# Optimization experiments

Hardware: AMD Instinct MI355X
Metric: run time of the kernel (lower is better)

The kernel has to match this reference:

```python
import jax, jax.numpy as jnp
import numpy as np

# Graph / model dims (match init_kwargs config)
N1, N2, N3 = 80000, 16000, 4096
E1, E2 = 256000, 65536
D_IN, H1, C1 = 256, 8, 64   # conv1: concat -> 512
H2, C2 = 4, 64              # conv2: mean over heads -> gnn_outdim=64
F_IN, F_HID, L_DIM, N_CLS = 128, 64, 64, 1


def setup_inputs() -> dict:
    key = jax.random.key(0)
    ks = jax.random.split(key, 20)
    rng = np.random.default_rng(0)

    def edges(E, n_src, n_dst):
        src = rng.integers(0, n_src, size=E)
        dst = rng.integers(0, n_dst, size=E)
        # avoid incidental self loops (PyG remove_self_loops); explicit ones added in conv
        src = np.where(src == dst, src + 1, src)
        return jnp.asarray(src, jnp.int32), jnp.asarray(dst, jnp.int32)

    es1, ed1 = edges(E1, N1, N2)
    es2, ed2 = edges(E2, N2, N3)
    s = 0.05
    return {
        "x": jax.random.normal(ks[0], (N1, D_IN), jnp.float32),
        "flat": jax.random.normal(ks[1], (N3, F_IN), jnp.float32),
        "last": jax.random.normal(ks[2], (N3, L_DIM), jnp.float32),
        "edge_src1": es1, "edge_dst1": ed1,
        "edge_src2": es2, "edge_dst2": ed2,
        "W1_src": jax.random.normal(ks[3], (D_IN, H1 * C1), jnp.float32) * s,
        "W1_dst": jax.random.normal(ks[4], (D_IN, H1 * C1), jnp.float32) * s,
        "att1_src": jax.random.normal(ks[5], (H1, C1), jnp.float32) * s,
        "att1_dst": jax.random.normal(ks[6], (H1, C1), jnp.float32) * s,
        "bias1": jax.random.normal(ks[7], (H1 * C1,), jnp.float32) * s,
        "W2_src": jax.random.normal(ks[8], (H1 * C1, H2 * C2), jnp.float32) * s,
        "W2_dst": jax.random.normal(ks[9], (H1 * C1, H2 * C2), jnp.float32) * s,
        "att2_src": jax.random.normal(ks[10], (H2, C2), jnp.float32) * s,
        "att2_dst": jax.random.normal(ks[11], (H2, C2), jnp.float32) * s,
        "bias2": jax.random.normal(ks[12], (C2,), jnp.float32) * s,
        "flat_W": jax.random.normal(ks[13], (F_IN, F_HID), jnp.float32) * s,
        "flat_b": jax.random.normal(ks[14], (F_HID,), jnp.float32) * s,
        "out_W": jax.random.normal(ks[15], (C2 + F_HID + L_DIM, N_CLS), jnp.float32) * s,
        "out_b": jax.random.normal(ks[16], (N_CLS,), jnp.float32) * s,
    }


def gat_conv(x_src, x_dst, src, dst, W_s, W_d, a_s, a_d, b, concat):
    """PyG bipartite GATConv (eval mode, add_self_loops=True, neg slope 0.2)."""
    H, C = a_s.shape
    Ns, Nd = x_src.shape[0], x_dst.shape[0]
    h_s = (x_src @ W_s).reshape(Ns, H, C)
    h_d = (x_dst @ W_d).reshape(Nd, H, C)
    sl = jnp.arange(Nd, dtype=src.dtype)
    src = jnp.concatenate([src, sl])  # self loops on target nodes
    dst = jnp.concatenate([dst, sl])
    e_s = jnp.einsum("nhc,hc->nh", h_s, a_s)  # [Ns,H]
    e_d = jnp.einsum("nhc,hc->nh", h_d, a_d)  # [Nd,H]
    alpha = jax.nn.leaky_relu(e_s[src] + e_d[dst], negative_slope=0.2)  # [E,H]
    amax = jax.ops.segment_max(alpha, dst, num_segments=Nd)[dst]
    ex = jnp.exp(alpha - amax)
    w = ex / jax.ops.segment_sum(ex, dst, num_segments=Nd)[dst]  # segment softmax
    msg = w[:, :, None] * h_s[src]  # [E,H,C]
    out = jax.ops.segment_sum(msg, dst, num_segments=Nd)  # [Nd,H,C]
    out = out.reshape(Nd, H * C) if concat else out.mean(axis=1)
    return out + b


def reference(x, flat, last, edge_src1, edge_dst1, edge_src2, edge_dst2,
              W1_src, W1_dst, att1_src, att1_dst, bias1,
              W2_src, W2_dst, att2_src, att2_dst, bias2,
              flat_W, flat_b, out_W, out_b):
    # eval mode: featdrop / attndrop / main_dropout are identity
    h = gat_conv(x, x[:N2], edge_src1, edge_dst1,
                 W1_src, W1_dst, att1_src, att1_dst, bias1, concat=True)
    h = jax.nn.elu(h)
    h = gat_conv(h, h[:N3], edge_src2, edge_dst2,
                 W2_src, W2_dst, att2_src, att2_dst, bias2, concat=False)
    f = flat @ flat_W + flat_b
    z = jnp.concatenate([h, f, last], axis=1)  # [N3, 64+64+64]
    return z @ out_W + out_b  # [N3, num_cls]
```

## Files before the change

kernel.cpp:

```cpp
#include <hip/hip_runtime.h>
#include <hip/hip_bf16.h>
#include <cstdio>

typedef __attribute__((ext_vector_type(8))) short short8;
typedef __attribute__((ext_vector_type(8))) _Float16 half8;
typedef __attribute__((ext_vector_type(2))) __fp16 fp16x2;
typedef __attribute__((ext_vector_type(4))) float f32x4;
typedef __attribute__((ext_vector_type(4))) unsigned int uint4v;
typedef __attribute__((ext_vector_type(2))) unsigned int uint2v;

#if defined(__has_builtin)
#if __has_builtin(__builtin_amdgcn_fdot2) && __has_builtin(__builtin_amdgcn_perm) && __has_builtin(__builtin_amdgcn_cvt_pkrtz)
#define USE_DOT2 1
#endif
#endif

__device__ __forceinline__ float bfu2f(unsigned short u) {
    return __uint_as_float(((unsigned)u) << 16);
}
__device__ __forceinline__ unsigned short f2bfu(float f) {
    __hip_bfloat16 b = __float2bfloat16(f);
    union { __hip_bfloat16 b; unsigned short u; } cv; cv.b = b;
    return cv.u;
}
__device__ __forceinline__ unsigned short f2hu(float f) {
    _Float16 h = (_Float16)f;
    union { _Float16 h; unsigned short u; } cv; cv.h = h;
    return cv.u;
}
__device__ __forceinline__ float hu2f(unsigned short u) {
    union { unsigned short u; _Float16 h; } cv; cv.u = u;
    return (float)cv.h;
}
#ifdef USE_DOT2
__device__ __forceinline__ unsigned pkw(float w0, float w1) {
    union { fp16x2 v; unsigned u; } cv;
    cv.v = __builtin_amdgcn_cvt_pkrtz(w0, w1);
    return cv.u;
}
__device__ __forceinline__ float fdot2acc(unsigned a, unsigned b, float c) {
    union { unsigned u; fp16x2 v; } ua, ub; ua.u = a; ub.u = b;
    return __builtin_amdgcn_fdot2(ua.v, ub.v, c, false);
}
#endif

#define N1 80000
#define N2 16000
#define N3 4096
#define E1 256000
#define E2 65536

__global__ void prep_hist(const float* __restrict__ W1s, unsigned short* __restrict__ w1s_pk,
                          const float* __restrict__ W2s, unsigned short* __restrict__ w2s_pk,
                          const float* __restrict__ W1d, const float* __restrict__ a1d,
                          float* __restrict__ v1dT,
                          const float* __restrict__ W2d, const float* __restrict__ a2d,
                          float* __restrict__ v2dT,
                          const float* __restrict__ fW, unsigned short* __restrict__ fw_t3,
                          int PB,
                          const int* __restrict__ ed1i, int* __restrict__ cnt1,
                          const int* __restrict__ ed2i, int* __restrict__ cnt2) {
    const int bid = blockIdx.x;
    if (bid < PB) {
        int i = bid * 256 + threadIdx.x;
        const int S0 = 131072, S1 = 131072, S2 = 8192;
        if (i < S0) {
            int k = i >> 9, n = i & 511;
            int n16 = n >> 4, l = n & 15, k32 = k >> 5, qq = (k >> 3) & 3, e = k & 7;
            size_t base = ((size_t)(n16 * 8 + k32)) * 512 + (qq * 16 + l) * 8 + e;
            w1s_pk[base] = f2hu(W1s[i]);
        } else if (i < S0 + S1) {
            int j = i - S0;
            int k = j >> 8, n = j & 255;
            int n16 = n >> 4, l = n & 15, k32 = k >> 5, qq = (k >> 3) & 3, e = k & 7;
            size_t base = ((size_t)(n16 * 16 + k32)) * 512 + (qq * 16 + l) * 8 + e;
            w2s_pk[base] = f2hu(W2s[j]);
        } else if (i < S0 + S1 + S2) {
            int j = i - S0 - S1;
            int k = j >> 6, n = j & 63;
            float v = fW[j];
            unsigned short h = f2bfu(v);
            unsigned short l = f2bfu(v - bfu2f(h));
            size_t base = (size_t)n * 384;
            fw_t3[base + k] = h;
            fw_t3[base + 128 + k] = l;
            fw_t3[base + 256 + k] = h;
        } else {
            int j = i - S0 - S1 - S2;
            if (j < 2048) {
                int h = j >> 8, k = j & 255;
                float s = 0.f;
                for (int c = 0; c < 64; c++) s += W1d[k * 512 + h * 64 + c] * a1d[h * 64 + c];
                v1dT[j] = s;
            } else if (j < 4096) {
                int jj = j - 2048;
                int h = jj >> 9, k = jj & 511;
                float s = 0.f;
                for (int c = 0; c < 64; c++) s += W2d[k * 256 + h * 64 + c] * a2d[h * 64 + c];
                v2dT[jj] = s;
            }
        }
    } else {
        int i = (bid - PB) * 256 + threadIdx.x;
        if (i < E1) {
            int d = ed1i[i];
            if ((unsigned)d < (unsigned)N2) atomicAdd(&cnt1[d], 1);
        } else if (i < E1 + E2) {
            int d = ed2i[i - E1];
            if ((unsigned)d < (unsigned)N3) atomicAdd(&cnt2[d], 1);
        }
    }
}

__global__ __launch_bounds__(1024)
void scan_dual(const int* __restrict__ c1, int* __restrict__ s1, int Nd1,
               const int* __restrict__ c2, int* __restrict__ s2, int Nd2) {
    const int* cnt = (blockIdx.x == 0) ? c1 : c2;
    int* start = (blockIdx.x == 0) ? s1 : s2;
    int Nd = (blockIdx.x == 0) ? Nd1 : Nd2;
    __shared__ int part[1024];
    int t = threadIdx.x;
    int k = (Nd + 1023) >> 10;
    int lo = t * k, hi = min(lo + k, Nd);
    if (lo > Nd) lo = Nd;
    int s = 0;
    for (int i = lo; i < hi; i++) s += cnt[i];
    part[t] = s;
    __syncthreads();
    for (int off = 1; off < 1024; off <<= 1) {
        int v = (t >= off) ? part[t - off] : 0;
        __syncthreads();
        part[t] += v;
        __syncthreads();
    }
    int run = (t > 0) ? part[t - 1] : 0;
    for (int i = lo; i < hi; i++) { start[i] = run; run += cnt[i]; }
    if (t == 1023) start[Nd] = part[1023];
}

__device__ __forceinline__ void fill_core(int fb,
        const int* __restrict__ sa1, const int* __restrict__ da1,
        const int* __restrict__ st1, int* __restrict__ cu1, int* __restrict__ cs1,
        const int* __restrict__ sa2, const int* __restrict__ da2,
        const int* __restrict__ st2, int* __restrict__ cu2, int* __restrict__ cs2) {
    int i = fb * 256 + threadIdx.x;
    const int *sa, *da, *st;
    int *cu, *cs;
    int Nd, Ns, e;
    if (i < E1) { sa = sa1; da = da1; st = st1; cu = cu1; cs = cs1; Nd = N2; Ns = N1; e = i; }
    else if (i < E1 + E2) { sa = sa2; da = da2; st = st2; cu = cu2; cs = cs2; Nd = N3; Ns = N2; e = i - E1; }
    else return;
    int d = da[e];
    if ((unsigned)d >= (unsigned)Nd) return;
    int p = atomicAdd(&cu[d], 1);
    int idx = st[d] + p;
    if (idx >= st[d + 1]) return;
    int s = sa[e];
    if ((unsigned)s >= (unsigned)Ns) s = 0;
    cs[idx] = s;
}

__device__ __forceinline__ void ed1_core(const float* __restrict__ x, const float* __restrict__ v1dT,
                                         float* __restrict__ ed1, int blk) {
    const int lane = threadIdx.x & 63;
    const int w = threadIdx.x >> 6;
    float4 vv[8];
#pragma unroll
    for (int h = 0; h < 8; h++) vv[h] = *(const float4*)&v1dT[h * 256 + lane * 4];
    for (int i = 0; i < 4; i++) {
        int d = blk * 16 + w * 4 + i;
        if (d >= N2) return;
        float4 xv = *(const float4*)&x[(size_t)d * 256 + lane * 4];
        float p[8];
#pragma unroll
        for (int h = 0; h < 8; h++)
            p[h] = xv.x * vv[h].x + xv.y * vv[h].y + xv.z * vv[h].z + xv.w * vv[h].w;
#pragma unroll
        for (int off = 1; off < 64; off <<= 1)
#pragma unroll
            for (int h = 0; h < 8; h++) p[h] += __shfl_xor(p[h], off);
        if (lane < 8) {
            int hh = lane;
            float a01 = (hh & 1) ? p[1] : p[0], a23 = (hh & 1) ? p[3] : p[2];
            float a45 = (hh & 1) ? p[5] : p[4], a67 = (hh & 1) ? p[7] : p[6];
            float b0 = (hh & 2) ? a23 : a01, b1 = (hh & 2) ? a67 : a45;
            ed1[d * 8 + hh] = (hh & 4) ? b1 : b0;
        }
    }
}
__device__ __forceinline__ void ed2_core(const unsigned short* __restrict__ xh,
                                         const float* __restrict__ v2dT,
                                         float* __restrict__ ed2, int blk) {
    const int lane = threadIdx.x & 63;
    const int w = threadIdx.x >> 6;
    float vv[4][8];
#pragma unroll
    for (int h = 0; h < 4; h++)
#pragma unroll
        for (int j = 0; j < 8; j++) vv[h][j] = v2dT[h * 512 + lane * 8 + j];
    for (int i = 0; i < 4; i++) {
        int d = blk * 16 + w * 4 + i;
        if (d >= N3) return;
        uint4v rw = *(const uint4v*)&xh[(size_t)d * 512 + lane * 8];
        const unsigned short* rb = (const unsigned short*)&rw;
        float xf[8];
#pragma unroll
        for (int j = 0; j < 8; j++) xf[j] = hu2f(rb[j]);
        float p[4];
#pragma unroll
        for (int h = 0; h < 4; h++) {
            float s = 0.f;
#pragma unroll
            for (int j = 0; j < 8; j++) s += xf[j] * vv[h][j];
            p[h] = s;
        }
#pragma unroll
        for (int off = 1; off < 64; off <<= 1)
#pragma unroll
            for (int h = 0; h < 4; h++) p[h] += __shfl_xor(p[h], off);
        if (lane < 4) {
            int hh = lane;
            float a01 = (hh & 1) ? p[1] : p[0], a23 = (hh & 1) ? p[3] : p[2];
            ed2[d * 4 + hh] = (hh & 2) ? a23 : a01;
        }
    }
}

template <bool AF16>
__device__ __forceinline__ void gemm_core(_Float16 (*As)[64][72],
              const void* __restrict__ Ax,
              const unsigned short* __restrict__ Bp, unsigned short* __restrict__ C,
              const float* __restrict__ att, float* __restrict__ es_out,
              int MT, int NB, int N, int K, int H, int hb) {
    const int xcd = hb & 7;
    const int sI = hb >> 3;
    const int mt = (sI / NB) * 8 + xcd;
    const int nb = sI % NB;
    if (mt >= MT) return;
    const int m0 = mt * 64;
    const int tid = threadIdx.x;
    const int wave = tid >> 6, lane = tid & 63;
    const int q = lane >> 4, l15 = lane & 15;
    const int n0 = nb * 256 + wave * 64;
    const int KS = K >> 6;
    const int KSB = K >> 5;
    const int arow = tid >> 2, ac16 = (tid & 3) * 16;
    const unsigned short* Bbase = Bp + (size_t)(n0 >> 4) * KSB * 512 + lane * 8;

    f32x4 acc[4][4] = {};
    half8 b[2][4];
    float4 s0, s1, s2, s3;
    half8 sh0, sh1;

    auto stageLoad = [&](int t) {
        if constexpr (AF16) {
            const _Float16* p = (const _Float16*)Ax + (size_t)(m0 + arow) * K + t * 64 + ac16;
            sh0 = *(const half8*)p;
            sh1 = *(const half8*)(p + 8);
        } else {
            const float* p = (const float*)Ax + (size_t)(m0 + arow) * K + t * 64 + ac16;
            s0 = *(const float4*)p;
            s1 = *(const float4*)(p + 4);
            s2 = *(const float4*)(p + 8);
            s3 = *(const float4*)(p + 12);
        }
    };
    auto stageWrite = [&](int buf) {
        half8 v0, v1;
        if constexpr (AF16) {
            v0 = sh0; v1 = sh1;
        } else {
            v0[0] = (_Float16)s0.x; v0[1] = (_Float16)s0.y;
            v0[2] = (_Float16)s0.z; v0[3] = (_Float16)s0.w;
            v0[4] = (_Float16)s1.x; v0[5] = (_Float16)s1.y;
            v0[6] = (_Float16)s1.z; v0[7] = (_Float16)s1.w;
            v1[0] = (_Float16)s2.x; v1[1] = (_Float16)s2.y;
            v1[2] = (_Float16)s2.z; v1[3] = (_Float16)s2.w;
            v1[4] = (_Float16)s3.x; v1[5] = (_Float16)s3.y;
            v1[6] = (_Float16)s3.z; v1[7] = (_Float16)s3.w;
        }
        *(half8*)&As[buf][arow][ac16] = v0;
        *(half8*)&As[buf][arow][ac16 + 8] = v1;
    };
    auto loadB = [&](int k32, int kh, int nt) {
        b[kh][nt] = *(const half8*)(Bbase + ((size_t)nt * KSB + k32) * 512);
    };

    stageLoad(0);
#pragma unroll
    for (int kh = 0; kh < 2; kh++)
#pragma unroll
        for (int nt = 0; nt < 4; nt++) loadB(kh, kh, nt);
    stageWrite(0);
    __syncthreads();

    int cur = 0;
    for (int t = 0; t < KS; t++) {
        const bool hn = (t + 1) < KS;
        if (hn) stageLoad(t + 1);
#pragma unroll
        for (int kh = 0; kh < 2; kh++) {
#pragma unroll
            for (int rg = 0; rg < 4; rg++) {
                half8 a = *(const half8*)&As[cur][rg * 16 + l15][kh * 32 + q * 8];
#pragma unroll
                for (int nt = 0; nt < 4; nt++) {
                    acc[rg][nt] = __builtin_amdgcn_mfma_f32_16x16x32_f16(a, b[kh][nt], acc[rg][nt], 0, 0, 0);
                    if (rg == 3 && hn) loadB(2 * (t + 1) + kh, kh, nt);
                }
            }
        }
        if (hn) {
            stageWrite(cur ^ 1);
            __syncthreads();
        }
        cur ^= 1;
    }

#pragma unroll
    for (int rg = 0; rg < 4; rg++)
#pragma unroll
        for (int nt = 0; nt < 4; nt++)
#pragma unroll
            for (int r = 0; r < 4; r++) {
                int row = m0 + rg * 16 + q * 4 + r;
                int col = n0 + nt * 16 + l15;
                C[(size_t)row * N + col] = f2hu(acc[rg][nt][r]);
            }
    {
        const int head = n0 >> 6;
        float av[4];
#pragma unroll
        for (int nt = 0; nt < 4; nt++) av[nt] = att[head * 64 + nt * 16 + l15];
#pragma unroll
        for (int rg = 0; rg < 4; rg++)
#pragma unroll
            for (int r = 0; r < 4; r++) {
                float p = acc[rg][0][r] * av[0] + acc[rg][1][r] * av[1]
                        + acc[rg][2][r] * av[2] + acc[rg][3][r] * av[3];
#pragma unroll
                for (int off = 1; off < 16; off <<= 1) p += __shfl_xor(p, off);
                if (l15 == 0)
                    es_out[(size_t)(m0 + rg * 16 + q * 4 + r) * H + head] = p;
            }
    }
}

__global__ __launch_bounds__(256, 2)
void gemm1_fused(const void* __restrict__ Ax,
                 const unsigned short* __restrict__ Bp, unsigned short* __restrict__ C,
                 const float* __restrict__ att, float* __restrict__ es_out,
                 int MT, int NB, int N, int K, int H, int G1, int FB,
                 const int* sa1, const int* da1, const int* st1, int* cu1, int* cs1,
                 const int* sa2, const int* da2, const int* st2, int* cu2, int* cs2,
                 const float* __restrict__ xe, const float* __restrict__ v1dT,
                 float* __restrict__ ed1) {
    __shared__ alignas(16) _Float16 As[2][64][72];
    const int bid = blockIdx.x;
    if (bid < G1) gemm_core<false>(As, Ax, Bp, C, att, es_out, MT, NB, N, K, H, bid);
    else if (bid < G1 + FB) fill_core(bid - G1, sa1, da1, st1, cu1, cs1, sa2, da2, st2, cu2, cs2);
    else ed1_core(xe, v1dT, ed1, bid - G1 - FB);
}

__device__ __forceinline__ void flat_core(unsigned char* smemraw,
        const float* __restrict__ A, const unsigned short* __restrict__ Bt3,
        float* __restrict__ C, int mb) {
    const int K = 128, N = 64, KK = 384;
    auto As = (unsigned short (*)[64][72])smemraw;
    auto Bs = (unsigned short (*)[72])(smemraw + 18432);
    const int tid = threadIdx.x;
    const int wave = tid >> 6, lane = tid & 63;
    const int wr = wave >> 1, wc = wave & 1;
    const int quad = lane >> 4, l15 = lane & 15;
    const int m0 = mb * 64, n0 = 0;
    f32x4 acc[2][2] = {};
    for (int k0 = 0; k0 < KK; k0 += 64) {
        const int seg = k0 / K;
        const int ks = k0 - seg * K;
#pragma unroll
        for (int i = 0; i < 2; i++) {
            int idx = tid + i * 256;
            int r = idx >> 3, cv = (idx & 7) * 8;
            const float* ap = &A[(size_t)(m0 + r) * K + ks + cv];
            const float4 v0 = *(const float4*)ap;
            const float4 v1 = *(const float4*)(ap + 4);
            float va[8] = {v0.x, v0.y, v0.z, v0.w, v1.x, v1.y, v1.z, v1.w};
            short8 h8, l8;
#pragma unroll
            for (int j = 0; j < 8; j++) {
                unsigned short hh = f2bfu(va[j]);
                h8[j] = (short)hh;
                l8[j] = (short)f2bfu(va[j] - bfu2f(hh));
            }
            *(short8*)&As[0][r][cv] = h8;
            *(short8*)&As[1][r][cv] = l8;
            *(short8*)&Bs[r][cv] = *(const short8*)&Bt3[(size_t)(n0 + r) * KK + k0 + cv];
        }
        __syncthreads();
        const int abank = (seg < 2) ? 0 : 1;
#pragma unroll
        for (int kk = 0; kk < 64; kk += 32) {
            short8 a[2], b[2];
#pragma unroll
            for (int t = 0; t < 2; t++) {
                a[t] = *(const short8*)&As[abank][wr * 32 + t * 16 + l15][kk + quad * 8];
                b[t] = *(const short8*)&Bs[wc * 32 + t * 16 + l15][kk + quad * 8];
            }
#pragma unroll
            for (int mt = 0; mt < 2; mt++)
#pragma unroll
                for (int nt = 0; nt < 2; nt++)
                    acc[mt][nt] = __builtin_amdgcn_mfma_f32_16x16x32_bf16(
                        a[mt], b[nt], acc[mt][nt], 0, 0, 0);
        }
        __syncthreads();
    }
#pragma unroll
    for (int mt = 0; mt < 2; mt++)
#pragma unroll
        for (int nt = 0; nt < 2; nt++)
#pragma unroll
            for (int r = 0; r < 4; r++) {
                int row = m0 + wr * 32 + mt * 16 + quad * 4 + r;
                int col = n0 + wc * 32 + nt * 16 + l15;
                C[(size_t)row * N + col] = acc[mt][nt][r];
            }
}

__global__ __launch_bounds__(256, 2)
void gemm2_fused(const void* __restrict__ Ax,
                 const unsigned short* __restrict__ Bp, unsigned short* __restrict__ C,
                 const float* __restrict__ att, float* __restrict__ es_out,
                 int MT, int NB, int N, int K, int H, int G2, int FLB,
                 const float* __restrict__ fA, const unsigned short* __restrict__ fBt3,
                 float* __restrict__ fC,
                 const unsigned short* __restrict__ x2h, const float* __restrict__ v2dT,
                 float* __restrict__ ed2) {
    __shared__ alignas(16) unsigned char smem[27648];
    const int bid = blockIdx.x;
    if (bid < G2) gemm_core<true>((_Float16(*)[64][72])smem, Ax, Bp, C, att, es_out,
                                  MT, NB, N, K, H, bid);
    else if (bid < G2 + FLB) flat_core(smem, fA, fBt3, fC, bid - G2);
    else ed2_core(x2h, v2dT, ed2, bid - G2 - FLB);
}

template <int H, bool ELU, bool HOUT, bool FIN>
__global__ __launch_bounds__(256)
void gat_agg3(const int* __restrict__ csr, const int* __restrict__ rs,
              const unsigned short* __restrict__ hs,
              const float* __restrict__ es,
              const float* __restrict__ edv,
              const float* __restrict__ bias,
              void* __restrict__ out, int Nd,
              const float* __restrict__ fbuf, const float* __restrict__ flat_b,
              const float* __restrict__ last, const float* __restrict__ outW,
              const float* __restrict__ outb, float* __restrict__ fout) {
    constexpr int LH = (H == 8) ? 3 : 2;
    constexpr int EPC = 64 >> LH;
    constexpr int ND = H / 2;
    const int lane = threadIdx.x & 63;
    const int d = blockIdx.x * 4 + (threadIdx.x >> 6);
    if (d >= Nd) return;
    const int h = lane & (H - 1);
    const int e0 = lane >> LH;
    const int hB = lane >> (6 - LH);
    const float edh = edv[(size_t)d * H + h];
    const int beg = rs[d];
    const int deg = rs[d + 1] - beg;
    const int n = deg + 1;
    const int nch = (n + EPC - 1) / EPC;
    float acc[H] = {};
    const size_t rowoff = (size_t)lane * H;
    if (nch <= 8) {
        int idxA = d, idxB = d;
        if (lane < deg) idxA = csr[beg + lane];
        if constexpr (H == 4) { if (64 + lane < deg) idxB = csr[beg + 64 + lane]; }
        float av[8];
#pragma unroll
        for (int c = 0; c < 8; c++) {
            if (c < nch) {
                int jv = c * EPC + e0;
                int s;
                if (c * EPC + EPC - 1 < 64) s = __shfl(idxA, jv);
                else s = __shfl(idxB, jv - 64);
                av[c] = es[(size_t)s * H + h];
            }
        }
        unsigned rvA[EPC][ND], rvB[EPC][ND];
        auto loadChunk = [&](int c, unsigned (&rv)[EPC][ND]) {
#pragma unroll
            for (int u = 0; u < EPC; u++) {
                int src = c * EPC + u;
                int s = (src < 64) ? __shfl(idxA, src) : __shfl(idxB, src - 64);
                const unsigned short* rp = &hs[(size_t)s * (H * 64) + rowoff];
                if constexpr (H == 8) *(uint4v*)&rv[u][0] = *(const uint4v*)rp;
                else *(uint2v*)&rv[u][0] = *(const uint2v*)rp;
            }
        };
        loadChunk(0, rvA);
        float al[8], mx = -1e30f;
#pragma unroll
        for (int c = 0; c < 8; c++) {
            int jv = c * EPC + e0;
            float a = -1e30f;
            if (c < nch && jv < n) { a = av[c] + edh; a = (a > 0.f) ? a : 0.2f * a; }
            al[c] = a;
            mx = fmaxf(mx, a);
        }
#pragma unroll
        for (int off = H; off < 64; off <<= 1) mx = fmaxf(mx, __shfl_xor(mx, off));
        float exv[8], den = 0.f;
#pragma unroll
        for (int c = 0; c < 8; c++) { exv[c] = expf(al[c] - mx); den += exv[c]; }
#pragma unroll
        for (int off = H; off < 64; off <<= 1) den += __shfl_xor(den, off);
        const float inv = 1.f / den;
        float ec[8];
#pragma unroll
        for (int c = 0; c < 8; c++) ec[c] = exv[c] * inv;
        auto computeChunk = [&](int c, unsigned (&rv)[EPC][ND]) {
#pragma unroll
            for (int pu = 0; pu < EPC / 2; pu++) {
                float w0 = __shfl(ec[c], (2 * pu) * H + hB);
                float w1 = __shfl(ec[c], (2 * pu + 1) * H + hB);
#ifdef USE_DOT2
                unsigned w2 = pkw(w0, w1);
#pragma unroll
                for (int dwi = 0; dwi < ND; dwi++) {
                    unsigned lo = __builtin_amdgcn_perm(rv[2 * pu + 1][dwi], rv[2 * pu][dwi], 0x05040100u);
                    unsigned hi = __builtin_amdgcn_perm(rv[2 * pu + 1][dwi], rv[2 * pu][dwi], 0x07060302u);
                    acc[2 * dwi] = fdot2acc(w2, lo, acc[2 * dwi]);
                    acc[2 * dwi + 1] = fdot2acc(w2, hi, acc[2 * dwi + 1]);
                }
#else
#pragma unroll
                for (int dwi = 0; dwi < ND; dwi++) {
                    unsigned q0 = rv[2 * pu][dwi], q1 = rv[2 * pu + 1][dwi];
                    acc[2 * dwi]     += w0 * hu2f((unsigned short)(q0 & 0xffff))
                                      + w1 * hu2f((unsigned short)(q1 & 0xffff));
                    acc[2 * dwi + 1] += w0 * hu2f((unsigned short)(q0 >> 16))
                                      + w1 * hu2f((unsigned short)(q1 >> 16));
                }
#endif
            }
        };
#pragma unroll
        for (int c = 0; c < 8; c += 2) {
            if (c >= nch) break;
            if (c + 1 < nch) loadChunk(c + 1, rvB);
            computeChunk(c, rvA);
            if (c + 1 >= nch) break;
            if (c + 2 < nch) loadChunk(c + 2, rvA);
            computeChunk(c + 1, rvB);
        }
    } else {
        float mx = -1e30f;
        for (int j0 = 0; j0 < n; j0 += EPC) {
            int j = j0 + e0;
            if (j < n) {
                int s = (j < deg) ? csr[beg + j] : d;
                float a = es[(size_t)s * H + h] + edh;
                a = (a > 0.0f) ? a : 0.2f * a;
                mx = fmaxf(mx, a);
            }
        }
#pragma unroll
        for (int off = H; off < 64; off <<= 1) mx = fmaxf(mx, __shfl_xor(mx, off));
        float den = 0.0f;
        for (int j0 = 0; j0 < n; j0 += EPC) {
            int j = j0 + e0;
            if (j < n) {
                int s = (j < deg) ? csr[beg + j] : d;
                float a = es[(size_t)s * H + h] + edh;
                a = (a > 0.0f) ? a : 0.2f * a;
                den += expf(a - mx);
            }
        }
#pragma unroll
        for (int off = H; off < 64; off <<= 1) den += __shfl_xor(den, off);
        const float inv = 1.0f / den;
        const float mB = __shfl(mx, hB);
        const float invB = __shfl(inv, hB);
        const float edhB = __shfl(edh, hB);
        for (int j = 0; j < n; j++) {
            int s = (j < deg) ? csr[beg + j] : d;
            const unsigned short* rp = &hs[(size_t)s * (H * 64) + rowoff];
            float a = es[(size_t)s * H + hB] + edhB;
            a = (a > 0.0f) ? a : 0.2f * a;
            float w = expf(a - mB) * invB;
#pragma unroll
            for (int k = 0; k < H; k++) acc[k] += w * hu2f(rp[k]);
        }
    }
    if constexpr (FIN) {
        float f4[4];
#pragma unroll
        for (int k = 0; k < 4; k++) {
            float a2v = acc[k] + __shfl_xor(acc[k], 32);
            f4[k] = a2v + __shfl_xor(a2v, 16);
        }
        float part = 0.f;
        if (lane < 16) {
            const int c0 = lane * 4;
            float4 fb4 = *(const float4*)&fbuf[(size_t)d * 64 + c0];
            float4 lb4 = *(const float4*)&last[(size_t)d * 64 + c0];
            const float* fbv = &fb4.x;
            const float* lbv = &lb4.x;
#pragma unroll
            for (int k = 0; k < 4; k++) {
                int c = c0 + k;
                float h2 = 0.25f * f4[k] + bias[c];
                part += h2 * outW[c];
                part += (fbv[k] + flat_b[c]) * outW[64 + c];
                part += lbv[k] * outW[128 + c];
            }
        }
#pragma unroll
        for (int off = 1; off < 16; off <<= 1) part += __shfl_xor(part, off);
        if (lane == 0) fout[d] = part + outb[0];
    } else {
#pragma unroll
        for (int k = 0; k < H; k++) {
            float v = acc[k];
            if (ELU) {
                v += bias[lane * H + k];
                v = (v > 0.0f) ? v : expm1f(v);
            }
            acc[k] = v;
        }
        if constexpr (HOUT) {
            half8 hv;
#pragma unroll
            for (int k = 0; k < H; k++) hv[k] = (_Float16)acc[k];
            _Float16* op = (_Float16*)out + (size_t)d * (H * 64) + rowoff;
            *(half8*)op = hv;
        } else {
            float* op = (float*)out + (size_t)d * (H * 64) + rowoff;
#pragma unroll
            for (int qd = 0; qd < H / 4; qd++)
                *(float4*)&op[qd * 4] = *(float4*)&acc[qd * 4];
        }
    }
}

extern "C" void kernel_launch(void* const* d_in, const int* in_sizes, int n_in,
                              void* d_out, int out_size, void* d_ws, size_t ws_size,
                              hipStream_t stream) {
    const float* x    = (const float*)d_in[0];
    const float* flat = (const float*)d_in[1];
    const float* last = (const float*)d_in[2];
    const int*  es1i  = (const int*)d_in[3];
    const int*  ed1i  = (const int*)d_in[4];
    const int*  es2i  = (const int*)d_in[5];
    const int*  ed2i  = (const int*)d_in[6];
    const float* W1s  = (const float*)d_in[7];
    const float* W1d  = (const float*)d_in[8];
    const float* a1s  = (const float*)d_in[9];
    const float* a1d  = (const float*)d_in[10];
    const float* b1   = (const float*)d_in[11];
    const float* W2s  = (const float*)d_in[12];
    const float* W2d  = (const float*)d_in[13];
    const float* a2s  = (const float*)d_in[14];
    const float* a2d  = (const float*)d_in[15];
    const float* b2   = (const float*)d_in[16];
    const float* fW   = (const float*)d_in[17];
    const float* fb   = (const float*)d_in[18];
    const float* oW   = (const float*)d_in[19];
    const float* ob   = (const float*)d_in[20];
    float* out = (float*)d_out;

    float* ws = (float*)d_ws;
    unsigned short* hs1_h = (unsigned short*)ws;
    float* es1f = ws + 24576000;
    float* ed1f = ws + 25216000;
    float* acc1 = ws + 25344000;
    unsigned short* wb = (unsigned short*)(ws + 54016000);
    unsigned short* w1s_pk = wb;
    unsigned short* w2s_pk = wb + 524288;
    unsigned short* fw_t3  = wb + 1048576;
    float* v1dT = ws + 54600000;
    float* v2dT = ws + 54602048;
    int* ibase   = (int*)(ws + 54816000);
    int* cnt1    = ibase;
    int* cursor1 = ibase + 16000;
    int* cnt2    = ibase + 32000;
    int* cursor2 = ibase + 36096;
    int* start1  = ibase + 40192;
    int* start2  = ibase + 56193;
    int* csr1    = ibase + 60290;
    int* csr2    = ibase + 316290;
    const size_t NEED = ((size_t)54816000 + 381826) * 4;
    if (ws_size < NEED) {
        fprintf(stderr, "kernel_launch: ws_size %zu < needed %zu\n", ws_size, NEED);
        return;
    }
    unsigned short* hs2_h = (unsigned short*)ws;
    float* es2f = ws + 2572288;
    float* ed2f = ws + 2636288;
    float* fbuf = ws + 3701248;
    unsigned short* acc1h = (unsigned short*)acc1;

    (void)hipMemsetAsync(ibase, 0, 40192 * sizeof(int), stream);
    {
        const int PB = 1072;
        const int HB = (E1 + E2) / 256;
        prep_hist<<<PB + HB, 256, 0, stream>>>(
            W1s, w1s_pk, W2s, w2s_pk,
            W1d, a1d, v1dT, W2d, a2d, v2dT,
            fW, fw_t3, PB, ed1i, cnt1, ed2i, cnt2);
    }
    scan_dual<<<2, 1024, 0, stream>>>(cnt1, start1, N2, cnt2, start2, N3);

    {
        const int MT = N1 / 64;
        const int NB = 2;
        const int G1 = 8 * NB * ((MT + 7) / 8);
        const int FB = (E1 + E2) / 256;
        const int EB = N2 / 16;
        gemm1_fused<<<G1 + FB + EB, 256, 0, stream>>>(
            x, w1s_pk, hs1_h, a1s, es1f, MT, NB, 512, 256, 8, G1, FB,
            es1i, ed1i, start1, cursor1, csr1, es2i, ed2i, start2, cursor2, csr2,
            x, v1dT, ed1f);
    }
    gat_agg3<8, true, true, false><<<N2 / 4, 256, 0, stream>>>(
        csr1, start1, hs1_h, es1f, ed1f, b1, acc1h, N2,
        nullptr, nullptr, nullptr, nullptr, nullptr, nullptr);

    {
        const int MT = N2 / 64;
        const int G2 = 8 * ((MT + 7) / 8);
        const int FLB = N3 / 64;
        const int EB2 = N3 / 16;
        gemm2_fused<<<G2 + FLB + EB2, 256, 0, stream>>>(
            acc1h, w2s_pk, hs2_h, a2s, es2f, MT, 1, 256, 512, 4, G2, FLB,
            flat, fw_t3, fbuf,
            acc1h, v2dT, ed2f);
    }
    gat_agg3<4, false, false, true><<<N3 / 4, 256, 0, stream>>>(
        csr2, start2, hs2_h, es2f, ed2f, b2, nullptr, N3,
        fbuf, fb, last, oW, ob, out);
}
```

Before: 322.4 us.

## Stage full-K A tile in LDS once and loop N passes per block

The GEMM core now loads the entire K-depth A tile into shared memory once, replacing the double-buffered K-step pipeline. For gemm1, one block computes both 256-column halves in two passes over the resident A tile, so x is read and converted once instead of by two blocks. For gemm2, the M tile shrinks to 32 rows with full K=512 resident, doubling block count. This removes redundant A reads and per-step barriers, but loses overlap of global loads with MFMA and increases LDS use, which may lower occupancy.

After: 326.3 us. No clear change (+1.2%).

```diff
diff --git a/kernel.cpp b/kernel.cpp
--- a/kernel.cpp
+++ b/kernel.cpp
@@ -226,123 +226,113 @@
     }
 }
 
-template <bool AF16>
-__device__ __forceinline__ void gemm_core(_Float16 (*As)[64][72],
+template <bool AF16, int MR, int KDIM, int NPASS, int PAD>
+__device__ __forceinline__ void gemm_core(_Float16* Ast,
               const void* __restrict__ Ax,
               const unsigned short* __restrict__ Bp, unsigned short* __restrict__ C,
               const float* __restrict__ att, float* __restrict__ es_out,
-              int MT, int NB, int N, int K, int H, int hb) {
+              int MT, int N, int H, int hb) {
+    constexpr int RG = MR / 16;
+    constexpr int KS = KDIM / 64;
+    constexpr int KSB = KDIM / 32;
     const int xcd = hb & 7;
-    const int sI = hb >> 3;
-    const int mt = (sI / NB) * 8 + xcd;
-    const int nb = sI % NB;
+    const int mt = (hb >> 3) * 8 + xcd;
     if (mt >= MT) return;
-    const int m0 = mt * 64;
+    const int m0 = mt * MR;
     const int tid = threadIdx.x;
     const int wave = tid >> 6, lane = tid & 63;
     const int q = lane >> 4, l15 = lane & 15;
-    const int n0 = nb * 256 + wave * 64;
-    const int KS = K >> 6;
-    const int KSB = K >> 5;
-    const int arow = tid >> 2, ac16 = (tid & 3) * 16;
-    const unsigned short* Bbase = Bp + (size_t)(n0 >> 4) * KSB * 512 + lane * 8;
-
-    f32x4 acc[4][4] = {};
-    half8 b[2][4];
-    float4 s0, s1, s2, s3;
-    half8 sh0, sh1;
-
-    auto stageLoad = [&](int t) {
-        if constexpr (AF16) {
-            const _Float16* p = (const _Float16*)Ax + (size_t)(m0 + arow) * K + t * 64 + ac16;
-            sh0 = *(const half8*)p;
-            sh1 = *(const half8*)(p + 8);
-        } else {
-            const float* p = (const float*)Ax + (size_t)(m0 + arow) * K + t * 64 + ac16;
-            s0 = *(const float4*)p;
-            s1 = *(const float4*)(p + 4);
-            s2 = *(const float4*)(p + 8);
-            s3 = *(const float4*)(p + 12);
-        }
-    };
-    auto stageWrite = [&](int buf) {
-        half8 v0, v1;
-        if constexpr (AF16) {
-            v0 = sh0; v1 = sh1;
-        } else {
-            v0[0] = (_Float16)s0.x; v0[1] = (_Float16)s0.y;
-            v0[2] = (_Float16)s0.z; v0[3] = (_Float16)s0.w;
-            v0[4] = (_Float16)s1.x; v0[5] = (_Float16)s1.y;
-            v0[6] = (_Float16)s1.z; v0[7] = (_Float16)s1.w;
-            v1[0] = (_Float16)s2.x; v1[1] = (_Float16)s2.y;
-            v1[2] = (_Float16)s2.z; v1[3] = (_Float16)s2.w;
-            v1[4] = (_Float16)s3.x; v1[5] = (_Float16)s3.y;
-            v1[6] = (_Float16)s3.z; v1[7] = (_Float16)s3.w;
-        }
-        *(half8*)&As[buf][arow][ac16] = v0;
-        *(half8*)&As[buf][arow][ac16 + 8] = v1;
-    };
-    auto loadB = [&](int k32, int kh, int nt) {
-        b[kh][nt] = *(const half8*)(Bbase + ((size_t)nt * KSB + k32) * 512);
-    };
-
-    stageLoad(0);
-#pragma unroll
-    for (int kh = 0; kh < 2; kh++)
-#pragma unroll
-        for (int nt = 0; nt < 4; nt++) loadB(kh, kh, nt);
-    stageWrite(0);
+
+    if constexpr (!AF16) {
+        const int srow = tid >> 2, scg = (tid & 3) * 64;
+        const float* sp = (const float*)Ax + (size_t)(m0 + srow) * KDIM + scg;
+        _Float16* dp = &Ast[srow * PAD + scg];
+#pragma unroll
+        for (int r = 0; r < 4; r++) {
+            float4 v0 = *(const float4*)(sp + r * 16);
+            float4 v1 = *(const float4*)(sp + r * 16 + 4);
+            float4 v2 = *(const float4*)(sp + r * 16 + 8);
+            float4 v3 = *(const float4*)(sp + r * 16 + 12);
+            half8 h0, h1;
+            h0[0] = (_Float16)v0.x; h0[1] = (_Float16)v0.y;
+            h0[2] = (_Float16)v0.z; h0[3] = (_Float16)v0.w;
+            h0[4] = (_Float16)v1.x; h0[5] = (_Float16)v1.y;
+            h0[6] = (_Float16)v1.z; h0[7] = (_Float16)v1.w;
+            h1[0] = (_Float16)v2.x; h1[1] = (_Float16)v2.y;
+            h1[2] = (_Float16)v2.z; h1[3] = (_Float16)v2.w;
+            h1[4] = (_Float16)v3.x; h1[5] = (_Float16)v3.y;
+            h1[6] = (_Float16)v3.z; h1[7] = (_Float16)v3.w;
+            *(half8*)(dp + r * 16) = h0;
+            *(half8*)(dp + r * 16 + 8) = h1;
+        }
+    } else {
+        const int srow = tid >> 3, scg = (tid & 7) * 64;
+        const _Float16* sp = (const _Float16*)Ax + (size_t)(m0 + srow) * KDIM + scg;
+        _Float16* dp = &Ast[srow * PAD + scg];
+#pragma unroll
+        for (int r = 0; r < 4; r++) {
+            half8 h0 = *(const half8*)(sp + r * 16);
+            half8 h1 = *(const half8*)(sp + r * 16 + 8);
+            *(half8*)(dp + r * 16) = h0;
+            *(half8*)(dp + r * 16 + 8) = h1;
+        }
+    }
     __syncthreads();
 
-    int cur = 0;
-    for (int t = 0; t < KS; t++) {
-        const bool hn = (t + 1) < KS;
-        if (hn) stageLoad(t + 1);
-#pragma unroll
-        for (int kh = 0; kh < 2; kh++) {
-#pragma unroll
-            for (int rg = 0; rg < 4; rg++) {
-                half8 a = *(const half8*)&As[cur][rg * 16 + l15][kh * 32 + q * 8];
-#pragma unroll
-                for (int nt = 0; nt < 4; nt++) {
-                    acc[rg][nt] = __builtin_amdgcn_mfma_f32_16x16x32_f16(a, b[kh][nt], acc[rg][nt], 0, 0, 0);
-                    if (rg == 3 && hn) loadB(2 * (t + 1) + kh, kh, nt);
+#pragma unroll
+    for (int np = 0; np < NPASS; np++) {
+        const int n0 = np * 256 + wave * 64;
+        const unsigned short* Bbase = Bp + (size_t)(n0 >> 4) * KSB * 512 + lane * 8;
+        f32x4 acc[RG][4] = {};
+        half8 b[2][4];
+        auto loadB = [&](int k32, int kh, int nt) {
+            b[kh][nt] = *(const half8*)(Bbase + ((size_t)nt * KSB + k32) * 512);
+        };
+#pragma unroll
+        for (int kh = 0; kh < 2; kh++)
+#pragma unroll
+            for (int nt = 0; nt < 4; nt++) loadB(kh, kh, nt);
+#pragma unroll
+        for (int t = 0; t < KS; t++) {
+#pragma unroll
+            for (int kh = 0; kh < 2; kh++)
+#pragma unroll
+                for (int rg = 0; rg < RG; rg++) {
+                    half8 a = *(const half8*)&Ast[(rg * 16 + l15) * PAD + t * 64 + kh * 32 + q * 8];
+#pragma unroll
+                    for (int nt = 0; nt < 4; nt++) {
+                        acc[rg][nt] = __builtin_amdgcn_mfma_f32_16x16x32_f16(a, b[kh][nt], acc[rg][nt], 0, 0, 0);
+                        if (rg == RG - 1 && t + 1 < KS) loadB(2 * (t + 1) + kh, kh, nt);
+                    }
                 }
-            }
-        }
-        if (hn) {
-            stageWrite(cur ^ 1);
-            __syncthreads();
-        }
-        cur ^= 1;
-    }
-
-#pragma unroll
-    for (int rg = 0; rg < 4; rg++)
-#pragma unroll
-        for (int nt = 0; nt < 4; nt++)
-#pragma unroll
-            for (int r = 0; r < 4; r++) {
-                int row = m0 + rg * 16 + q * 4 + r;
-                int col = n0 + nt * 16 + l15;
-                C[(size_t)row * N + col] = f2hu(acc[rg][nt][r]);
-            }
-    {
-        const int head = n0 >> 6;
-        float av[4];
-#pragma unroll
-        for (int nt = 0; nt < 4; nt++) av[nt] = att[head * 64 + nt * 16 + l15];
-#pragma unroll
-        for (int rg = 0; rg < 4; rg++)
-#pragma unroll
-            for (int r = 0; r < 4; r++) {
-                float p = acc[rg][0][r] * av[0] + acc[rg][1][r] * av[1]
-                        + acc[rg][2][r] * av[2] + acc[rg][3][r] * av[3];
-#pragma unroll
-                for (int off = 1; off < 16; off <<= 1) p += __shfl_xor(p, off);
-                if (l15 == 0)
-                    es_out[(size_t)(m0 + rg * 16 + q * 4 + r) * H + head] = p;
-            }
+        }
+#pragma unroll
+        for (int rg = 0; rg < RG; rg++)
+#pragma unroll
+            for (int nt = 0; nt < 4; nt++)
+#pragma unroll
+                for (int r = 0; r < 4; r++) {
+                    int row = m0 + rg * 16 + q * 4 + r;
+                    int col = n0 + nt * 16 + l15;
+                    C[(size_t)row * N + col] = f2hu(acc[rg][nt][r]);
+                }
+        {
+            const int head = n0 >> 6;
+            float av[4];
+#pragma unroll
+            for (int nt = 0; nt < 4; nt++) av[nt] = att[head * 64 + nt * 16 + l15];
+#pragma unroll
+            for (int rg = 0; rg < RG; rg++)
+#pragma unroll
+                for (int r = 0; r < 4; r++) {
+                    float p = acc[rg][0][r] * av[0] + acc[rg][1][r] * av[1]
+                            + acc[rg][2][r] * av[2] + acc[rg][3][r] * av[3];
+#pragma unroll
+                    for (int off = 1; off < 16; off <<= 1) p += __shfl_xor(p, off);
+                    if (l15 == 0)
+                        es_out[(size_t)(m0 + rg * 16 + q * 4 + r) * H + head] = p;
+                }
+        }
     }
 }
 
@@ -350,14 +340,14 @@
 void gemm1_fused(const void* __restrict__ Ax,
                  const unsigned short* __restrict__ Bp, unsigned short* __restrict__ C,
                  const float* __restrict__ att, float* __restrict__ es_out,
-                 int MT, int NB, int N, int K, int H, int G1, int FB,
+                 int MT, int N, int H, int G1, int FB,
                  const int* sa1, const int* da1, const int* st1, int* cu1, int* cs1,
                  const int* sa2, const int* da2, const int* st2, int* cu2, int* cs2,
                  const float* __restrict__ xe, const float* __restrict__ v1dT,
                  float* __restrict__ ed1) {
-    __shared__ alignas(16) _Float16 As[2][64][72];
+    __shared__ alignas(16) _Float16 Ast[64 * 264];
     const int bid = blockIdx.x;
-    if (bid < G1) gemm_core<false>(As, Ax, Bp, C, att, es_out, MT, NB, N, K, H, bid);
+    if (bid < G1) gemm_core<false, 64, 256, 2, 264>(Ast, Ax, Bp, C, att, es_out, MT, N, H, bid);
     else if (bid < G1 + FB) fill_core(bid - G1, sa1, da1, st1, cu1, cs1, sa2, da2, st2, cu2, cs2);
     else ed1_core(xe, v1dT, ed1, bid - G1 - FB);
 }
@@ -431,15 +421,15 @@
 void gemm2_fused(const void* __restrict__ Ax,
                  const unsigned short* __restrict__ Bp, unsigned short* __restrict__ C,
                  const float* __restrict__ att, float* __restrict__ es_out,
-                 int MT, int NB, int N, int K, int H, int G2, int FLB,
+                 int MT, int N, int H, int G2, int FLB,
                  const float* __restrict__ fA, const unsigned short* __restrict__ fBt3,
                  float* __restrict__ fC,
                  const unsigned short* __restrict__ x2h, const float* __restrict__ v2dT,
                  float* __restrict__ ed2) {
-    __shared__ alignas(16) unsigned char smem[27648];
+    __shared__ alignas(16) unsigned char smem[33280];
     const int bid = blockIdx.x;
-    if (bid < G2) gemm_core<true>((_Float16(*)[64][72])smem, Ax, Bp, C, att, es_out,
-                                  MT, NB, N, K, H, bid);
+    if (bid < G2) gemm_core<true, 32, 512, 1, 520>((_Float16*)smem, Ax, Bp, C, att, es_out,
+                                                   MT, N, H, bid);
     else if (bid < G2 + FLB) flat_core(smem, fA, fBt3, fC, bid - G2);
     else ed2_core(x2h, v2dT, ed2, bid - G2 - FLB);
 }
@@ -713,12 +703,11 @@
 
     {
         const int MT = N1 / 64;
-        const int NB = 2;
-        const int G1 = 8 * NB * ((MT + 7) / 8);
+        const int G1 = 8 * ((MT + 7) / 8);
         const int FB = (E1 + E2) / 256;
         const int EB = N2 / 16;
         gemm1_fused<<<G1 + FB + EB, 256, 0, stream>>>(
-            x, w1s_pk, hs1_h, a1s, es1f, MT, NB, 512, 256, 8, G1, FB,
+            x, w1s_pk, hs1_h, a1s, es1f, MT, 512, 8, G1, FB,
             es1i, ed1i, start1, cursor1, csr1, es2i, ed2i, start2, cursor2, csr2,
             x, v1dT, ed1f);
     }
@@ -727,12 +716,12 @@
         nullptr, nullptr, nullptr, nullptr, nullptr, nullptr);
 
     {
-        const int MT = N2 / 64;
+        const int MT = N2 / 32;
         const int G2 = 8 * ((MT + 7) / 8);
         const int FLB = N3 / 64;
         const int EB2 = N3 / 16;
         gemm2_fused<<<G2 + FLB + EB2, 256, 0, stream>>>(
-            acc1h, w2s_pk, hs2_h, a2s, es2f, MT, 1, 256, 512, 4, G2, FLB,
+            acc1h, w2s_pk, hs2_h, a2s, es2f, MT, 256, 4, G2, FLB,
             flat, fw_t3, fbuf,
             acc1h, v2dT, ed2f);
     }
```
